# Optimization experiments

Hardware: AMD Instinct MI355X
Metric: run time of the kernel (lower is better)

The kernel has to match this reference:

```python
import jax, jax.numpy as jnp
import numpy as np

N_NODES = 100000
N_EDGES = 3200000
D_IN = 128
D_OUT = 128


def setup_inputs() -> dict:
    key = jax.random.key(0)
    k1, k2, k3, k4, k5, k6, k7, k8 = jax.random.split(key, 8)
    edge_row = jax.random.randint(k1, (N_EDGES,), 0, N_NODES, dtype=jnp.int64 if jax.config.jax_enable_x64 else jnp.int32)
    edge_col = jax.random.randint(k2, (N_EDGES,), 0, N_NODES, dtype=jnp.int64 if jax.config.jax_enable_x64 else jnp.int32)
    edge_val = jax.random.uniform(k3, (N_EDGES,), dtype=jnp.float32)
    X = jax.random.normal(k4, (N_NODES, D_IN), dtype=jnp.float32)
    s_in = 1.0 / np.sqrt(D_IN)
    W_pass = jax.random.normal(k5, (D_OUT, D_IN), dtype=jnp.float32) * s_in
    b_pass = jax.random.normal(k6, (D_OUT,), dtype=jnp.float32) * s_in
    W_self = jax.random.normal(k7, (D_OUT, D_IN), dtype=jnp.float32) * s_in
    b_self = jax.random.normal(k8, (D_OUT,), dtype=jnp.float32) * s_in
    return {"edge_row": edge_row, "edge_col": edge_col, "edge_val": edge_val,
            "X": X, "W_pass": W_pass, "b_pass": b_pass,
            "W_self": W_self, "b_self": b_self}


def reference(edge_row, edge_col, edge_val, X, W_pass, b_pass, W_self, b_self):
    # SpMM: (A @ X)[i] = sum_e{row[e]==i} val[e] * X[col[e]]
    gathered = edge_val[:, None] * X[edge_col]          # [E, D_in] gather
    agg = jax.ops.segment_sum(gathered, edge_row, num_segments=N_NODES)  # [N, D_in]
    # pass_map(A @ X) + self_map(X)
    return agg @ W_pass.T + b_pass + X @ W_self.T + b_self
```

## Files before the change

kernel.cpp:

```cpp
#include <hip/hip_runtime.h>

#define NN 100000
#define NE 3200000
#define ROWS_PB 98
#define NBUCK 1021
#define ESTRIDE 3584
#define P1_EDGES 8192
#define BIN_BLOCKS 391
#define XCAST_BLOCKS 3125
#define FRONT_GRID (BIN_BLOCKS + XCAST_BLOCKS)
#define XQ_SCALE (127.f / 6.f)
#define XQ_INV   (6.f / (127.f * 255.f))

typedef float f4 __attribute__((ext_vector_type(4)));
typedef short bf8 __attribute__((ext_vector_type(8)));

static __device__ __forceinline__ unsigned f2bf(float f) {
  unsigned u = __float_as_uint(f);
  return (u + 0x7FFFu + ((u >> 16) & 1u)) >> 16;
}


__global__ __launch_bounds__(256) void k_init_pack(const float* __restrict__ Wp,
                                                   const float* __restrict__ Ws,
                                                   const float* __restrict__ bp,
                                                   const float* __restrict__ bs,
                                                   int* __restrict__ gcur,
                                                   short* __restrict__ Bfrag,
                                                   float* __restrict__ bias) {
  int idx = blockIdx.x * 256 + threadIdx.x;
  if (idx < NBUCK) gcur[idx] = idx * ESTRIDE;
  if (idx < 64 * 64) {
    int fid = idx >> 6, l = idx & 63;
    int kbi = fid >> 3, ci = fid & 7;
    int n = ci * 16 + (l & 15);
    bf8 pk;
#pragma unroll
    for (int b = 0; b < 8; b++) {
      int k = kbi * 32 + ((l >> 4) << 3) + b;
      float f = (k < 128) ? Wp[n * 128 + k] : Ws[n * 128 + (k - 128)];
      pk[b] = (short)f2bf(f);
    }
    *(bf8*)(Bfrag + (size_t)idx * 8) = pk;
  }
  if (idx < 128) bias[idx] = bp[idx] + bs[idx];
}


__global__ __launch_bounds__(512) void k_front(const int* __restrict__ erow,
                                               const int* __restrict__ ecol,
                                               const float* __restrict__ eval,
                                               const float* __restrict__ X,
                                               int* __restrict__ gcur,
                                               unsigned* __restrict__ epk,
                                               char* __restrict__ xq8,
                                               char* __restrict__ ob) {
  __shared__ unsigned stg[P1_EDGES];
  __shared__ unsigned short keyarr[P1_EDGES];
  __shared__ int hist[NBUCK];
  __shared__ int cur[NBUCK];
  __shared__ int adj[NBUCK];
  __shared__ int s2[512];
  const int t = threadIdx.x;
  const int bid = blockIdx.x;

  if (bid >= BIN_BLOCKS) {
    int idx = (bid - BIN_BLOCKS) * 512 + t;
    int i = idx >> 4, c = idx & 15;
    const float* xp = X + (size_t)i * 128 + c * 8;
    f4 x0 = *(const f4*)xp;
    f4 x1 = *(const f4*)(xp + 4);
    uint4 o;
    o.x = f2bf(x0[0]) | (f2bf(x0[1]) << 16);
    o.y = f2bf(x0[2]) | (f2bf(x0[3]) << 16);
    o.z = f2bf(x1[0]) | (f2bf(x1[1]) << 16);
    o.w = f2bf(x1[2]) | (f2bf(x1[3]) << 16);
    *(uint4*)(ob + (size_t)i * 512 + c * 16) = o;
    unsigned q[8];
#pragma unroll
    for (int j = 0; j < 8; j++) {
      float v = (j < 4) ? x0[j] : x1[j - 4];
      float r = rintf(v * XQ_SCALE);
      r = fminf(fmaxf(r, -127.f), 127.f);
      q[j] = (unsigned)((int)r) & 0xFFu;
    }
    uint2 qo;
    qo.x = q[0] | (q[1] << 8) | (q[2] << 16) | (q[3] << 24);
    qo.y = q[4] | (q[5] << 8) | (q[6] << 16) | (q[7] << 24);
    *(uint2*)(xq8 + (size_t)i * 128 + c * 8) = qo;
    return;
  }

  const int e0 = bid * P1_EDGES;
  int rem = NE - e0;
  const int ec = rem < P1_EDGES ? rem : P1_EDGES;

  for (int i = t; i < NBUCK; i += 512) hist[i] = 0;
  __syncthreads();
  for (int i = t; i < ec; i += 512) atomicAdd(&hist[erow[e0 + i] / ROWS_PB], 1);
  __syncthreads();
  int h0 = (2 * t < NBUCK) ? hist[2 * t] : 0;
  int h1 = (2 * t + 1 < NBUCK) ? hist[2 * t + 1] : 0;
  s2[t] = h0 + h1;
  __syncthreads();
  for (int off = 1; off < 512; off <<= 1) {
    int x = (t >= off) ? s2[t - off] : 0;
    __syncthreads();
    s2[t] += x;
    __syncthreads();
  }
  int exp_ = s2[t] - (h0 + h1);
  if (2 * t < NBUCK) cur[2 * t] = exp_;
  if (2 * t + 1 < NBUCK) cur[2 * t + 1] = exp_ + h0;
  __syncthreads();
  for (int b = t; b < NBUCK; b += 512) {
    int c = hist[b];
    if (c) adj[b] = atomicAdd(&gcur[b], c) - cur[b];
  }
  __syncthreads();
  for (int i = t; i < ec; i += 512) {
    int r = erow[e0 + i];
    unsigned c = (unsigned)ecol[e0 + i];
    float v = eval[e0 + i];
    int bk = r / ROWS_PB;
    int rl = r - bk * ROWS_PB;
    unsigned vq = (unsigned)(v * 255.f + 0.5f);
    int pos = atomicAdd(&cur[bk], 1);
    stg[pos] = ((unsigned)rl << 25) | (c << 8) | vq;
    keyarr[pos] = (unsigned short)bk;
  }
  __syncthreads();
  for (int i = t; i < ec; i += 512) {
    int k = keyarr[i];
    int slot = adj[k] + i;
    if (slot < (k + 1) * ESTRIDE)
      epk[slot] = stg[i];
  }
}


__global__ __launch_bounds__(512) void k_spmm(const int* __restrict__ gcur,
                                              const unsigned* __restrict__ epk,
                                              const char* __restrict__ xq8,
                                              char* __restrict__ ob) {
  __shared__ unsigned raw[ESTRIDE];
  __shared__ unsigned stg[ESTRIDE];
  __shared__ int sc[128];
  __shared__ int rbeg[ROWS_PB + 1];
  __shared__ int cur[ROWS_PB];
  const int t = threadIdx.x;
  const int l = t & 63;
  const int wv = t >> 6;
  const int b = blockIdx.x;
  const int base = b * ESTRIDE;
  int ec = gcur[b] - base;
  if (ec > ESTRIDE) ec = ESTRIDE;

  if (t < 128) sc[t] = 0;
  __syncthreads();
  for (int i = t; i < ec; i += 512) {
    unsigned p = epk[base + i];
    raw[i] = p;
    atomicAdd(&sc[p >> 25], 1);
  }
  __syncthreads();
  for (int off = 1; off < 128; off <<= 1) {
    int x = 0;
    if (t < 128 && t >= off) x = sc[t - off];
    __syncthreads();
    if (t < 128) sc[t] += x;
    __syncthreads();
  }
  if (t <= ROWS_PB) rbeg[t] = (t == 0) ? 0 : sc[t - 1];
  if (t < ROWS_PB) cur[t] = (t == 0) ? 0 : sc[t - 1];
  __syncthreads();
  for (int i = t; i < ec; i += 512) {
    unsigned p = raw[i];
    int pos = atomicAdd(&cur[p >> 25], 1);
    stg[pos] = p;
  }
  __syncthreads();

  const int row0 = b * ROWS_PB;
  const int lb = l * 2;
  for (int r = wv; r < ROWS_PB; r += 8) {
    const int row = row0 + r;
    if (row >= NN) break;
    int e = rbeg[r];
    const int e2 = rbeg[r + 1];
    int ax = 0, ay = 0;
    for (; e + 8 <= e2; e += 8) {
      unsigned p0 = __builtin_amdgcn_readfirstlane(stg[e]);
      unsigned p1 = __builtin_amdgcn_readfirstlane(stg[e + 1]);
      unsigned p2 = __builtin_amdgcn_readfirstlane(stg[e + 2]);
      unsigned p3 = __builtin_amdgcn_readfirstlane(stg[e + 3]);
      unsigned p4 = __builtin_amdgcn_readfirstlane(stg[e + 4]);
      unsigned p5 = __builtin_amdgcn_readfirstlane(stg[e + 5]);
      unsigned p6 = __builtin_amdgcn_readfirstlane(stg[e + 6]);
      unsigned p7 = __builtin_amdgcn_readfirstlane(stg[e + 7]);
      char2 x0 = *(const char2*)(xq8 + (size_t)((p0 >> 8) & 0x1FFFF) * 128 + lb);
      char2 x1 = *(const char2*)(xq8 + (size_t)((p1 >> 8) & 0x1FFFF) * 128 + lb);
      char2 x2 = *(const char2*)(xq8 + (size_t)((p2 >> 8) & 0x1FFFF) * 128 + lb);
      char2 x3 = *(const char2*)(xq8 + (size_t)((p3 >> 8) & 0x1FFFF) * 128 + lb);
      char2 x4 = *(const char2*)(xq8 + (size_t)((p4 >> 8) & 0x1FFFF) * 128 + lb);
      char2 x5 = *(const char2*)(xq8 + (size_t)((p5 >> 8) & 0x1FFFF) * 128 + lb);
      char2 x6 = *(const char2*)(xq8 + (size_t)((p6 >> 8) & 0x1FFFF) * 128 + lb);
      char2 x7 = *(const char2*)(xq8 + (size_t)((p7 >> 8) & 0x1FFFF) * 128 + lb);
      ax += (int)(p0 & 255u) * x0.x; ay += (int)(p0 & 255u) * x0.y;
      ax += (int)(p1 & 255u) * x1.x; ay += (int)(p1 & 255u) * x1.y;
      ax += (int)(p2 & 255u) * x2.x; ay += (int)(p2 & 255u) * x2.y;
      ax += (int)(p3 & 255u) * x3.x; ay += (int)(p3 & 255u) * x3.y;
      ax += (int)(p4 & 255u) * x4.x; ay += (int)(p4 & 255u) * x4.y;
      ax += (int)(p5 & 255u) * x5.x; ay += (int)(p5 & 255u) * x5.y;
      ax += (int)(p6 & 255u) * x6.x; ay += (int)(p6 & 255u) * x6.y;
      ax += (int)(p7 & 255u) * x7.x; ay += (int)(p7 & 255u) * x7.y;
    }
    for (; e + 2 <= e2; e += 2) {
      unsigned p0 = __builtin_amdgcn_readfirstlane(stg[e]);
      unsigned p1 = __builtin_amdgcn_readfirstlane(stg[e + 1]);
      char2 x0 = *(const char2*)(xq8 + (size_t)((p0 >> 8) & 0x1FFFF) * 128 + lb);
      char2 x1 = *(const char2*)(xq8 + (size_t)((p1 >> 8) & 0x1FFFF) * 128 + lb);
      ax += (int)(p0 & 255u) * x0.x; ay += (int)(p0 & 255u) * x0.y;
      ax += (int)(p1 & 255u) * x1.x; ay += (int)(p1 & 255u) * x1.y;
    }
    if (e < e2) {
      unsigned p0 = __builtin_amdgcn_readfirstlane(stg[e]);
      char2 x0 = *(const char2*)(xq8 + (size_t)((p0 >> 8) & 0x1FFFF) * 128 + lb);
      ax += (int)(p0 & 255u) * x0.x; ay += (int)(p0 & 255u) * x0.y;
    }
    float fx = (float)ax * XQ_INV, fy = (float)ay * XQ_INV;
    unsigned o = f2bf(fx) | (f2bf(fy) << 16);
    *(unsigned*)(ob + (size_t)row * 512 + 256 + l * 4) = o;
  }
}


__global__ __launch_bounds__(256) void k_gemm(const char* __restrict__ ab,
                                              const short* __restrict__ Bfrag,
                                              const float* __restrict__ bias,
                                              float* __restrict__ out) {
  const int t = threadIdx.x;
  const int w = t >> 6, l = t & 63;
  const int i0 = blockIdx.x * 128 + w * 32;
  const int lm = l & 15, lk = l >> 4;

  f4 acc[2][8];
#pragma unroll
  for (int mi = 0; mi < 2; mi++)
#pragma unroll
    for (int ci = 0; ci < 8; ci++) acc[mi][ci] = (f4){0.f, 0.f, 0.f, 0.f};

  int r0 = i0 + lm;       if (r0 > NN - 1) r0 = NN - 1;
  int r1 = i0 + 16 + lm;  if (r1 > NN - 1) r1 = NN - 1;
  const bf8* __restrict__ bfp = (const bf8*)Bfrag;

#pragma unroll
  for (int kb = 0; kb < 8; kb++) {
    const int off = (kb < 4) ? (256 + kb * 64) : ((kb - 4) * 64);
    bf8 a0 = *(const bf8*)(ab + (size_t)r0 * 512 + off + lk * 16);
    bf8 a1 = *(const bf8*)(ab + (size_t)r1 * 512 + off + lk * 16);
#pragma unroll
    for (int ci = 0; ci < 8; ci++) {
      bf8 b = bfp[(size_t)(kb * 8 + ci) * 64 + l];
      acc[0][ci] = __builtin_amdgcn_mfma_f32_16x16x32_bf16(a0, b, acc[0][ci], 0, 0, 0);
      acc[1][ci] = __builtin_amdgcn_mfma_f32_16x16x32_bf16(a1, b, acc[1][ci], 0, 0, 0);
    }
  }

#pragma unroll
  for (int ci = 0; ci < 8; ci++) {
    int col = ci * 16 + lm;
    float bv = bias[col];
#pragma unroll
    for (int mi = 0; mi < 2; mi++) {
      int rbase = i0 + mi * 16 + lk * 4;
#pragma unroll
      for (int r = 0; r < 4; r++) {
        int row = rbase + r;
        if (row < NN) out[(size_t)row * 128 + col] = acc[mi][ci][r] + bv;
      }
    }
  }
}


extern "C" void kernel_launch(void* const* d_in, const int* in_sizes, int n_in,
                              void* d_out, int out_size, void* d_ws, size_t ws_size,
                              hipStream_t stream) {
  (void)in_sizes; (void)n_in; (void)out_size; (void)ws_size;
  const int*   erow = (const int*)d_in[0];
  const int*   ecol = (const int*)d_in[1];
  const float* eval = (const float*)d_in[2];
  const float* X    = (const float*)d_in[3];
  const float* Wp   = (const float*)d_in[4];
  const float* bp   = (const float*)d_in[5];
  const float* Ws   = (const float*)d_in[6];
  const float* bs   = (const float*)d_in[7];
  float* out = (float*)d_out;

  char* ws = (char*)d_ws;
  size_t off = 0;
  auto alloc = [&](size_t bytes) -> void* {
    void* p = ws + off;
    off = (off + bytes + 255) & ~(size_t)255;
    return p;
  };
  unsigned* epk   = (unsigned*)alloc((size_t)NBUCK * ESTRIDE * 4);
  char*     xq8   = (char*)alloc((size_t)NN * 128);
  int*      gcur  = (int*)alloc((size_t)NBUCK * 4);
  short*    Bfrag = (short*)alloc((size_t)64 * 64 * 8 * 2);
  float*    bias  = (float*)alloc(128 * 4);

  hipLaunchKernelGGL(k_init_pack, dim3(17), dim3(256), 0, stream, Wp, Ws, bp, bs, gcur, Bfrag, bias);
  hipLaunchKernelGGL(k_front, dim3(FRONT_GRID), dim3(512), 0, stream,
                     erow, ecol, eval, X, gcur, epk, xq8, (char*)d_out);
  hipLaunchKernelGGL(k_spmm, dim3(NBUCK), dim3(512), 0, stream, gcur, epk, xq8, (char*)d_out);
  hipLaunchKernelGGL(k_gemm, dim3((NN + 127) / 128), dim3(256), 0, stream,
                     (const char*)d_out, Bfrag, bias, out);
}
```

Measured before the change: 140.5 us.

## Fuse SpMM aggregation with the dense GEMM epilogue into one kernel

Merges the SpMM and GEMM kernels. Each block keeps its aggregated bf16 rows in shared memory, and seven waves then run the MFMA GEMM over those rows plus the bf16 X half that is already stored in the output buffer. This removes one kernel launch and the global write and re-read of the aggregation. The raw shared staging array is also dropped, and edges are re-read from global memory instead. The cost is more shared memory per block, which may lower occupancy. The GEMM also writes fp32 output into the same rows it reads the X half from, which relies on per-row read-before-write ordering within a block.

Result: slower. 157.2 us (+11.9%).

```diff
diff --git a/kernel.cpp b/kernel.cpp
--- a/kernel.cpp
+++ b/kernel.cpp
@@ -139,12 +139,14 @@
 }
 
 
-__global__ __launch_bounds__(512) void k_spmm(const int* __restrict__ gcur,
-                                              const unsigned* __restrict__ epk,
-                                              const char* __restrict__ xq8,
-                                              char* __restrict__ ob) {
-  __shared__ unsigned raw[ESTRIDE];
+__global__ __launch_bounds__(512) void k_sg(const int* __restrict__ gcur,
+                                            const unsigned* __restrict__ epk,
+                                            const char* __restrict__ xq8,
+                                            const short* __restrict__ Bfrag,
+                                            const float* __restrict__ bias,
+                                            char* __restrict__ ob) {
   __shared__ unsigned stg[ESTRIDE];
+  __shared__ unsigned agg[112 * 68];
   __shared__ int sc[128];
   __shared__ int rbeg[ROWS_PB + 1];
   __shared__ int cur[ROWS_PB];
@@ -158,11 +160,7 @@
 
   if (t < 128) sc[t] = 0;
   __syncthreads();
-  for (int i = t; i < ec; i += 512) {
-    unsigned p = epk[base + i];
-    raw[i] = p;
-    atomicAdd(&sc[p >> 25], 1);
-  }
+  for (int i = t; i < ec; i += 512) atomicAdd(&sc[epk[base + i] >> 25], 1);
   __syncthreads();
   for (int off = 1; off < 128; off <<= 1) {
     int x = 0;
@@ -175,7 +173,7 @@
   if (t < ROWS_PB) cur[t] = (t == 0) ? 0 : sc[t - 1];
   __syncthreads();
   for (int i = t; i < ec; i += 512) {
-    unsigned p = raw[i];
+    unsigned p = epk[base + i];
     int pos = atomicAdd(&cur[p >> 25], 1);
     stg[pos] = p;
   }
@@ -184,8 +182,7 @@
   const int row0 = b * ROWS_PB;
   const int lb = l * 2;
   for (int r = wv; r < ROWS_PB; r += 8) {
-    const int row = row0 + r;
-    if (row >= NN) break;
+    if (row0 + r >= NN) break;
     int e = rbeg[r];
     const int e2 = rbeg[r + 1];
     int ax = 0, ay = 0;
@@ -229,55 +226,41 @@
       ax += (int)(p0 & 255u) * x0.x; ay += (int)(p0 & 255u) * x0.y;
     }
     float fx = (float)ax * XQ_INV, fy = (float)ay * XQ_INV;
-    unsigned o = f2bf(fx) | (f2bf(fy) << 16);
-    *(unsigned*)(ob + (size_t)row * 512 + 256 + l * 4) = o;
-  }
-}
-
-
-__global__ __launch_bounds__(256) void k_gemm(const char* __restrict__ ab,
-                                              const short* __restrict__ Bfrag,
-                                              const float* __restrict__ bias,
-                                              float* __restrict__ out) {
-  const int t = threadIdx.x;
-  const int w = t >> 6, l = t & 63;
-  const int i0 = blockIdx.x * 128 + w * 32;
-  const int lm = l & 15, lk = l >> 4;
-
-  f4 acc[2][8];
-#pragma unroll
-  for (int mi = 0; mi < 2; mi++)
-#pragma unroll
-    for (int ci = 0; ci < 8; ci++) acc[mi][ci] = (f4){0.f, 0.f, 0.f, 0.f};
-
-  int r0 = i0 + lm;       if (r0 > NN - 1) r0 = NN - 1;
-  int r1 = i0 + 16 + lm;  if (r1 > NN - 1) r1 = NN - 1;
-  const bf8* __restrict__ bfp = (const bf8*)Bfrag;
-
-#pragma unroll
-  for (int kb = 0; kb < 8; kb++) {
-    const int off = (kb < 4) ? (256 + kb * 64) : ((kb - 4) * 64);
-    bf8 a0 = *(const bf8*)(ab + (size_t)r0 * 512 + off + lk * 16);
-    bf8 a1 = *(const bf8*)(ab + (size_t)r1 * 512 + off + lk * 16);
+    agg[r * 68 + l] = f2bf(fx) | (f2bf(fy) << 16);
+  }
+  __syncthreads();
+
+  if (wv < 7) {
+    const int lm = l & 15, lk = l >> 4;
+    const int lrow = wv * 16 + lm;
+    int growc = row0 + lrow;
+    if (growc > NN - 1) growc = NN - 1;
+    f4 acc[8];
+#pragma unroll
+    for (int ci = 0; ci < 8; ci++) acc[ci] = (f4){0.f, 0.f, 0.f, 0.f};
+    const bf8* __restrict__ bfp = (const bf8*)Bfrag;
+    const char* aggp = (const char*)agg + lrow * 272;
+    const char* xhp = ob + (size_t)growc * 512;
+#pragma unroll
+    for (int kb = 0; kb < 8; kb++) {
+      bf8 a = (kb < 4) ? *(const bf8*)(aggp + kb * 64 + lk * 16)
+                       : *(const bf8*)(xhp + (kb - 4) * 64 + lk * 16);
+#pragma unroll
+      for (int ci = 0; ci < 8; ci++) {
+        bf8 bb = bfp[(size_t)(kb * 8 + ci) * 64 + l];
+        acc[ci] = __builtin_amdgcn_mfma_f32_16x16x32_bf16(a, bb, acc[ci], 0, 0, 0);
+      }
+    }
 #pragma unroll
     for (int ci = 0; ci < 8; ci++) {
-      bf8 b = bfp[(size_t)(kb * 8 + ci) * 64 + l];
-      acc[0][ci] = __builtin_amdgcn_mfma_f32_16x16x32_bf16(a0, b, acc[0][ci], 0, 0, 0);
-      acc[1][ci] = __builtin_amdgcn_mfma_f32_16x16x32_bf16(a1, b, acc[1][ci], 0, 0, 0);
-    }
-  }
-
-#pragma unroll
-  for (int ci = 0; ci < 8; ci++) {
-    int col = ci * 16 + lm;
-    float bv = bias[col];
-#pragma unroll
-    for (int mi = 0; mi < 2; mi++) {
-      int rbase = i0 + mi * 16 + lk * 4;
+      int col = ci * 16 + lm;
+      float bv = bias[col];
 #pragma unroll
       for (int r = 0; r < 4; r++) {
-        int row = rbase + r;
-        if (row < NN) out[(size_t)row * 128 + col] = acc[mi][ci][r] + bv;
+        int lr = wv * 16 + lk * 4 + r;
+        int grow = row0 + lr;
+        if (lr < ROWS_PB && grow < NN)
+          *(float*)(ob + (size_t)grow * 512 + col * 4) = acc[ci][r] + bv;
       }
     }
   }
@@ -296,7 +279,6 @@
   const float* bp   = (const float*)d_in[5];
   const float* Ws   = (const float*)d_in[6];
   const float* bs   = (const float*)d_in[7];
-  float* out = (float*)d_out;
 
   char* ws = (char*)d_ws;
   size_t off = 0;
@@ -314,7 +296,6 @@
   hipLaunchKernelGGL(k_init_pack, dim3(17), dim3(256), 0, stream, Wp, Ws, bp, bs, gcur, Bfrag, bias);
   hipLaunchKernelGGL(k_front, dim3(FRONT_GRID), dim3(512), 0, stream,
                      erow, ecol, eval, X, gcur, epk, xq8, (char*)d_out);
-  hipLaunchKernelGGL(k_spmm, dim3(NBUCK), dim3(512), 0, stream, gcur, epk, xq8, (char*)d_out);
-  hipLaunchKernelGGL(k_gemm, dim3((NN + 127) / 128), dim3(256), 0, stream,
-                     (const char*)d_out, Bfrag, bias, out);
-}
+  hipLaunchKernelGGL(k_sg, dim3(NBUCK), dim3(512), 0, stream,
+                     gcur, epk, xq8, Bfrag, bias, (char*)d_out);
+}
```

## Sort SpMM edges by column chunk then row for gather locality

Applied to the files above, without the earlier changes.

The SpMM kernel now buckets each block's edges by (column chunk of 16K nodes, local row) rather than by row alone. All 8 waves then sweep the chunks in lockstep, keeping 13 per-row accumulators in registers. The aim is to confine concurrent gathers of the int8 X rows to a 2MB window so they hit in L2/MALL. The cost is a 4x larger shared-memory histogram and scan, a second global read of epk in place of the shared raw copy, shorter inner loops, and more registers.

New measurement: 173.1 us. 23.2% more time.

```diff
diff --git a/kernel.cpp b/kernel.cpp
--- a/kernel.cpp
+++ b/kernel.cpp
@@ -11,6 +11,9 @@
 #define FRONT_GRID (BIN_BLOCKS + XCAST_BLOCKS)
 #define XQ_SCALE (127.f / 6.f)
 #define XQ_INV   (6.f / (127.f * 255.f))
+#define CSHIFT 14
+#define NCHUNK 7
+#define NKEY (NCHUNK * 128)
 
 typedef float f4 __attribute__((ext_vector_type(4)));
 typedef short bf8 __attribute__((ext_vector_type(8)));
@@ -143,11 +146,11 @@
                                               const unsigned* __restrict__ epk,
                                               const char* __restrict__ xq8,
                                               char* __restrict__ ob) {
-  __shared__ unsigned raw[ESTRIDE];
   __shared__ unsigned stg[ESTRIDE];
-  __shared__ int sc[128];
-  __shared__ int rbeg[ROWS_PB + 1];
-  __shared__ int cur[ROWS_PB];
+  __shared__ int sc[NKEY];
+  __shared__ int rbeg[NKEY + 1];
+  __shared__ int cur[NKEY];
+  __shared__ int s2[512];
   const int t = threadIdx.x;
   const int l = t & 63;
   const int wv = t >> 6;
@@ -156,81 +159,84 @@
   int ec = gcur[b] - base;
   if (ec > ESTRIDE) ec = ESTRIDE;
 
-  if (t < 128) sc[t] = 0;
+  for (int i = t; i < NKEY; i += 512) sc[i] = 0;
   __syncthreads();
   for (int i = t; i < ec; i += 512) {
     unsigned p = epk[base + i];
-    raw[i] = p;
-    atomicAdd(&sc[p >> 25], 1);
-  }
-  __syncthreads();
-  for (int off = 1; off < 128; off <<= 1) {
-    int x = 0;
-    if (t < 128 && t >= off) x = sc[t - off];
+    int key = (int)(((p >> 8) & 0x1FFFF) >> CSHIFT) * 128 + (int)(p >> 25);
+    atomicAdd(&sc[key], 1);
+  }
+  __syncthreads();
+  int h0 = (2 * t < NKEY) ? sc[2 * t] : 0;
+  int h1 = (2 * t + 1 < NKEY) ? sc[2 * t + 1] : 0;
+  s2[t] = h0 + h1;
+  __syncthreads();
+  for (int off = 1; off < 512; off <<= 1) {
+    int x = (t >= off) ? s2[t - off] : 0;
     __syncthreads();
-    if (t < 128) sc[t] += x;
+    s2[t] += x;
     __syncthreads();
   }
-  if (t <= ROWS_PB) rbeg[t] = (t == 0) ? 0 : sc[t - 1];
-  if (t < ROWS_PB) cur[t] = (t == 0) ? 0 : sc[t - 1];
+  int exc = s2[t] - (h0 + h1);
+  if (2 * t < NKEY) { rbeg[2 * t] = exc; cur[2 * t] = exc; }
+  if (2 * t + 1 < NKEY) { rbeg[2 * t + 1] = exc + h0; cur[2 * t + 1] = exc + h0; }
+  if (t == 511) rbeg[NKEY] = s2[511];
   __syncthreads();
   for (int i = t; i < ec; i += 512) {
-    unsigned p = raw[i];
-    int pos = atomicAdd(&cur[p >> 25], 1);
+    unsigned p = epk[base + i];
+    int key = (int)(((p >> 8) & 0x1FFFF) >> CSHIFT) * 128 + (int)(p >> 25);
+    int pos = atomicAdd(&cur[key], 1);
     stg[pos] = p;
   }
   __syncthreads();
 
   const int row0 = b * ROWS_PB;
   const int lb = l * 2;
-  for (int r = wv; r < ROWS_PB; r += 8) {
-    const int row = row0 + r;
-    if (row >= NN) break;
-    int e = rbeg[r];
-    const int e2 = rbeg[r + 1];
-    int ax = 0, ay = 0;
-    for (; e + 8 <= e2; e += 8) {
-      unsigned p0 = __builtin_amdgcn_readfirstlane(stg[e]);
-      unsigned p1 = __builtin_amdgcn_readfirstlane(stg[e + 1]);
-      unsigned p2 = __builtin_amdgcn_readfirstlane(stg[e + 2]);
-      unsigned p3 = __builtin_amdgcn_readfirstlane(stg[e + 3]);
-      unsigned p4 = __builtin_amdgcn_readfirstlane(stg[e + 4]);
-      unsigned p5 = __builtin_amdgcn_readfirstlane(stg[e + 5]);
-      unsigned p6 = __builtin_amdgcn_readfirstlane(stg[e + 6]);
-      unsigned p7 = __builtin_amdgcn_readfirstlane(stg[e + 7]);
-      char2 x0 = *(const char2*)(xq8 + (size_t)((p0 >> 8) & 0x1FFFF) * 128 + lb);
-      char2 x1 = *(const char2*)(xq8 + (size_t)((p1 >> 8) & 0x1FFFF) * 128 + lb);
-      char2 x2 = *(const char2*)(xq8 + (size_t)((p2 >> 8) & 0x1FFFF) * 128 + lb);
-      char2 x3 = *(const char2*)(xq8 + (size_t)((p3 >> 8) & 0x1FFFF) * 128 + lb);
-      char2 x4 = *(const char2*)(xq8 + (size_t)((p4 >> 8) & 0x1FFFF) * 128 + lb);
-      char2 x5 = *(const char2*)(xq8 + (size_t)((p5 >> 8) & 0x1FFFF) * 128 + lb);
-      char2 x6 = *(const char2*)(xq8 + (size_t)((p6 >> 8) & 0x1FFFF) * 128 + lb);
-      char2 x7 = *(const char2*)(xq8 + (size_t)((p7 >> 8) & 0x1FFFF) * 128 + lb);
-      ax += (int)(p0 & 255u) * x0.x; ay += (int)(p0 & 255u) * x0.y;
-      ax += (int)(p1 & 255u) * x1.x; ay += (int)(p1 & 255u) * x1.y;
-      ax += (int)(p2 & 255u) * x2.x; ay += (int)(p2 & 255u) * x2.y;
-      ax += (int)(p3 & 255u) * x3.x; ay += (int)(p3 & 255u) * x3.y;
-      ax += (int)(p4 & 255u) * x4.x; ay += (int)(p4 & 255u) * x4.y;
-      ax += (int)(p5 & 255u) * x5.x; ay += (int)(p5 & 255u) * x5.y;
-      ax += (int)(p6 & 255u) * x6.x; ay += (int)(p6 & 255u) * x6.y;
-      ax += (int)(p7 & 255u) * x7.x; ay += (int)(p7 & 255u) * x7.y;
-    }
-    for (; e + 2 <= e2; e += 2) {
-      unsigned p0 = __builtin_amdgcn_readfirstlane(stg[e]);
-      unsigned p1 = __builtin_amdgcn_readfirstlane(stg[e + 1]);
-      char2 x0 = *(const char2*)(xq8 + (size_t)((p0 >> 8) & 0x1FFFF) * 128 + lb);
-      char2 x1 = *(const char2*)(xq8 + (size_t)((p1 >> 8) & 0x1FFFF) * 128 + lb);
-      ax += (int)(p0 & 255u) * x0.x; ay += (int)(p0 & 255u) * x0.y;
-      ax += (int)(p1 & 255u) * x1.x; ay += (int)(p1 & 255u) * x1.y;
-    }
-    if (e < e2) {
-      unsigned p0 = __builtin_amdgcn_readfirstlane(stg[e]);
-      char2 x0 = *(const char2*)(xq8 + (size_t)((p0 >> 8) & 0x1FFFF) * 128 + lb);
-      ax += (int)(p0 & 255u) * x0.x; ay += (int)(p0 & 255u) * x0.y;
-    }
-    float fx = (float)ax * XQ_INV, fy = (float)ay * XQ_INV;
-    unsigned o = f2bf(fx) | (f2bf(fy) << 16);
-    *(unsigned*)(ob + (size_t)row * 512 + 256 + l * 4) = o;
+  int ax[13], ay[13];
+#pragma unroll
+  for (int ri = 0; ri < 13; ri++) { ax[ri] = 0; ay[ri] = 0; }
+
+  for (int c = 0; c < NCHUNK; c++) {
+#pragma unroll
+    for (int ri = 0; ri < 13; ri++) {
+      const int r = wv + ri * 8;
+      if (r < ROWS_PB) {
+        int e = rbeg[c * 128 + r];
+        const int e2 = rbeg[c * 128 + r + 1];
+        int a0 = ax[ri], a1 = ay[ri];
+        for (; e + 4 <= e2; e += 4) {
+          unsigned p0 = __builtin_amdgcn_readfirstlane(stg[e]);
+          unsigned p1 = __builtin_amdgcn_readfirstlane(stg[e + 1]);
+          unsigned p2 = __builtin_amdgcn_readfirstlane(stg[e + 2]);
+          unsigned p3 = __builtin_amdgcn_readfirstlane(stg[e + 3]);
+          char2 x0 = *(const char2*)(xq8 + (size_t)((p0 >> 8) & 0x1FFFF) * 128 + lb);
+          char2 x1 = *(const char2*)(xq8 + (size_t)((p1 >> 8) & 0x1FFFF) * 128 + lb);
+          char2 x2 = *(const char2*)(xq8 + (size_t)((p2 >> 8) & 0x1FFFF) * 128 + lb);
+          char2 x3 = *(const char2*)(xq8 + (size_t)((p3 >> 8) & 0x1FFFF) * 128 + lb);
+          a0 += (int)(p0 & 255u) * x0.x; a1 += (int)(p0 & 255u) * x0.y;
+          a0 += (int)(p1 & 255u) * x1.x; a1 += (int)(p1 & 255u) * x1.y;
+          a0 += (int)(p2 & 255u) * x2.x; a1 += (int)(p2 & 255u) * x2.y;
+          a0 += (int)(p3 & 255u) * x3.x; a1 += (int)(p3 & 255u) * x3.y;
+        }
+        for (; e < e2; e++) {
+          unsigned p0 = __builtin_amdgcn_readfirstlane(stg[e]);
+          char2 x0 = *(const char2*)(xq8 + (size_t)((p0 >> 8) & 0x1FFFF) * 128 + lb);
+          a0 += (int)(p0 & 255u) * x0.x; a1 += (int)(p0 & 255u) * x0.y;
+        }
+        ax[ri] = a0; ay[ri] = a1;
+      }
+    }
+  }
+
+#pragma unroll
+  for (int ri = 0; ri < 13; ri++) {
+    int r = wv + ri * 8;
+    int row = row0 + r;
+    if (r < ROWS_PB && row < NN) {
+      float fx = (float)ax[ri] * XQ_INV, fy = (float)ay[ri] * XQ_INV;
+      unsigned o = f2bf(fx) | (f2bf(fy) << 16);
+      *(unsigned*)(ob + (size_t)row * 512 + 256 + l * 4) = o;
+    }
   }
 }
 
```
